# Kernel tuning notes

Hardware: AMD Instinct MI355X
Metric: run time of the kernel (lower is better)

The kernel has to match this reference:

```python
import jax, jax.numpy as jnp
import numpy as np

B, TE, TD, H = 8, 512, 256, 256  # batch, enc len, dec len, hidden (He==Hd)

def setup_inputs() -> dict:
    key = jax.random.key(0)
    k1, k2, k3, k4, k5 = jax.random.split(key, 5)
    # Keras 'uniform' initializer: U(-0.05, 0.05)
    u = lambda k, s: jax.random.uniform(k, s, jnp.float32, -0.05, 0.05)
    return {
        "encoder_out_seq": jax.random.normal(k1, (B, TE, H), jnp.float32),
        "decoder_out_seq": jax.random.normal(k2, (B, TD, H), jnp.float32),
        "W_a": u(k3, (H, H)),
        "U_a": u(k4, (H, H)),
        "V_a": u(k5, (H, 1)),
    }

def reference(encoder_out_seq, decoder_out_seq, W_a, U_a, V_a):
    # Bahdanau additive attention, fully batched (same math as the per-step K.rnn loop)
    We = jnp.einsum('bih,hk->bik', encoder_out_seq, W_a)   # [B,Te,H]
    Uh = jnp.einsum('bjh,hk->bjk', decoder_out_seq, U_a)   # [B,Td,H]
    # energies: V_a^T tanh(We_i + Uh_j)  -> [B,Td,Te]
    t = jnp.tanh(We[:, None, :, :] + Uh[:, :, None, :])    # [B,Td,Te,H]
    e = jnp.einsum('bjih,h->bji', t, V_a[:, 0])             # [B,Td,Te]
    e = jax.nn.softmax(e, axis=-1)                          # softmax over encoder positions
    c = jnp.einsum('bji,bih->bjh', e, encoder_out_seq)      # [B,Td,H]
    return (c, e)
```

## Files before the change

### kernel.cpp

```cpp
#include <hip/hip_runtime.h>


#define BB 8
#define TE 512
#define TD 256
#define HH 256

#define EXP2F(x) __builtin_amdgcn_exp2f(x)
#define RCPF(x)  __builtin_amdgcn_rcpf(x)
#define KSCALE   2.8853900817779268f
#define NSC      (-2.8853900817779268f)

typedef _Float16 h4 __attribute__((ext_vector_type(4)));
typedef _Float16 h8 __attribute__((ext_vector_type(8)));

__global__ __launch_bounds__(256) void k_pre(
    const float* __restrict__ enc, const float* __restrict__ dec,
    const float* __restrict__ Wa,  const float* __restrict__ Ua,
    _Float16* __restrict__ W4h, float* __restrict__ Uhe,
    _Float16* __restrict__ enc16)
{
    const int tid = threadIdx.x;

    if (blockIdx.x >= 384) {
        const size_t base = (size_t)(blockIdx.x - 384) * 16384;
        #pragma unroll 4
        for (int t = 0; t < 16; t++) {
            size_t idx = base + ((size_t)t * 256 + tid) * 4;
            float4 v = *(const float4*)(enc + idx);
            h4 o; o.x = (_Float16)v.x; o.y = (_Float16)v.y;
            o.z = (_Float16)v.z; o.w = (_Float16)v.w;
            *(h4*)(enc16 + idx) = o;
        }
        return;
    }

    const bool is_enc = blockIdx.x < 256;
    const int bi = is_enc ? blockIdx.x : (blockIdx.x - 256);
    const int m0 = (bi >> 2) * 64;
    const int n0 = (bi & 3) * 64;
    const float* X = is_enc ? enc : dec;
    const float* W = is_enc ? Wa : Ua;

    __shared__ float Xs[32][68];
    __shared__ float Ws[32][68];

    const int kq = tid & 7,  xr = tid >> 3;
    const int wk = tid >> 3, wn = (tid & 7) * 8;
    const int tx = tid & 15, ty = tid >> 4;

    float acc[4][4];
    #pragma unroll
    for (int r = 0; r < 4; r++)
        #pragma unroll
        for (int c = 0; c < 4; c++) acc[r][c] = 0.f;

    for (int kc = 0; kc < HH; kc += 32) {
        float4 xa = *(const float4*)(X + (size_t)(m0 + xr) * HH + kc + kq * 4);
        float4 xb = *(const float4*)(X + (size_t)(m0 + xr + 32) * HH + kc + kq * 4);
        float4 wa = *(const float4*)(W + (size_t)(kc + wk) * HH + n0 + wn);
        float4 wb = *(const float4*)(W + (size_t)(kc + wk) * HH + n0 + wn + 4);
        __syncthreads();
        Xs[kq * 4 + 0][xr] = xa.x; Xs[kq * 4 + 1][xr] = xa.y;
        Xs[kq * 4 + 2][xr] = xa.z; Xs[kq * 4 + 3][xr] = xa.w;
        Xs[kq * 4 + 0][xr + 32] = xb.x; Xs[kq * 4 + 1][xr + 32] = xb.y;
        Xs[kq * 4 + 2][xr + 32] = xb.z; Xs[kq * 4 + 3][xr + 32] = xb.w;
        *(float4*)&Ws[wk][wn]     = wa;
        *(float4*)&Ws[wk][wn + 4] = wb;
        __syncthreads();
        #pragma unroll
        for (int k = 0; k < 32; k++) {
            float4 a = *(const float4*)&Xs[k][ty * 4];
            float4 b = *(const float4*)&Ws[k][tx * 4];
            acc[0][0] = fmaf(a.x, b.x, acc[0][0]); acc[0][1] = fmaf(a.x, b.y, acc[0][1]);
            acc[0][2] = fmaf(a.x, b.z, acc[0][2]); acc[0][3] = fmaf(a.x, b.w, acc[0][3]);
            acc[1][0] = fmaf(a.y, b.x, acc[1][0]); acc[1][1] = fmaf(a.y, b.y, acc[1][1]);
            acc[1][2] = fmaf(a.y, b.z, acc[1][2]); acc[1][3] = fmaf(a.y, b.w, acc[1][3]);
            acc[2][0] = fmaf(a.z, b.x, acc[2][0]); acc[2][1] = fmaf(a.z, b.y, acc[2][1]);
            acc[2][2] = fmaf(a.z, b.z, acc[2][2]); acc[2][3] = fmaf(a.z, b.w, acc[2][3]);
            acc[3][0] = fmaf(a.w, b.x, acc[3][0]); acc[3][1] = fmaf(a.w, b.y, acc[3][1]);
            acc[3][2] = fmaf(a.w, b.z, acc[3][2]); acc[3][3] = fmaf(a.w, b.w, acc[3][3]);
        }
    }

    if (is_enc) {
        const int b  = m0 >> 9;
        const int ib = (m0 & 511) + ty * 4;
        const int hh = n0 + tx * 4;
        const int o  = hh >> 3;
        const int hf = (hh & 7);
        #pragma unroll
        for (int r = 0; r < 4; r++) {
            h4 v;
            v.x = (_Float16)EXP2F(acc[r][0] * KSCALE);
            v.y = (_Float16)EXP2F(acc[r][1] * KSCALE);
            v.z = (_Float16)EXP2F(acc[r][2] * KSCALE);
            v.w = (_Float16)EXP2F(acc[r][3] * KSCALE);
            *(h4*)(W4h + (((size_t)b * 32 + o) * TE + ib + r) * 8 + hf) = v;
        }
    } else {
        #pragma unroll
        for (int r = 0; r < 4; r++) {
            float4 v;
            v.x = EXP2F(acc[r][0] * KSCALE); v.y = EXP2F(acc[r][1] * KSCALE);
            v.z = EXP2F(acc[r][2] * KSCALE); v.w = EXP2F(acc[r][3] * KSCALE);
            *(float4*)(Uhe + (size_t)(m0 + ty * 4 + r) * HH + n0 + tx * 4) = v;
        }
    }
}

__global__ __launch_bounds__(512) void k_attn(
    const _Float16* __restrict__ enc16, const _Float16* __restrict__ W4h,
    const float* __restrict__ Uhe, const float* __restrict__ Va,
    float* __restrict__ out_c, float* __restrict__ out_e)
{
    const int wv = threadIdx.x >> 6, lane = threadIdx.x & 63;
    const int b   = blockIdx.x & 7;
    const int j0  = (blockIdx.x >> 3) * 4;
    const int jj0 = b * TD + j0;

    __shared__ float sP[4][TE];
    __shared__ float sR[8][4][HH];

    const int i = (wv << 6) + lane;
    const _Float16* wp = W4h + ((size_t)b * 32 * TE + i) * 8;
    const float* ua = Uhe + (size_t)jj0 * HH;
    const float* va = Va;

    float a0 = 0.f, a1 = 0.f, a2 = 0.f, a3 = 0.f;

#define OSTEP(ACC, UA, UB)                                                \
    {                                                                     \
        float A0 = fmaf(w0, (UA).x, 1.f);                                 \
        float A1 = fmaf(w1, (UA).y, 1.f);                                 \
        float A2 = fmaf(w2, (UA).z, 1.f);                                 \
        float A3 = fmaf(w3, (UA).w, 1.f);                                 \
        float A4 = fmaf(w4, (UB).x, 1.f);                                 \
        float A5 = fmaf(w5, (UB).y, 1.f);                                 \
        float A6 = fmaf(w6, (UB).z, 1.f);                                 \
        float A7 = fmaf(w7, (UB).w, 1.f);                                 \
        float dab = A0 * A1, dcd = A2 * A3;                               \
        float def_ = A4 * A5, dgh = A6 * A7;                              \
        float nab = fmaf(v4a.x, A1, v4a.y * A0);                          \
        float ncd = fmaf(v4a.z, A3, v4a.w * A2);                          \
        float nef = fmaf(v4b.x, A5, v4b.y * A4);                          \
        float ngh = fmaf(v4b.z, A7, v4b.w * A6);                          \
        float den4a = dab * dcd,  den4b = def_ * dgh;                     \
        float num4a = fmaf(nab, dcd, ncd * dab);                          \
        float num4b = fmaf(nef, dgh, ngh * def_);                         \
        float num = fmaf(num4a, den4b, num4b * den4a);                    \
        ACC = fmaf(num, RCPF(den4a * den4b), ACC);                        \
    }

    #pragma unroll 2
    for (int q = 0; q < 32; q++) {
        h8 w8 = *(const h8*)(wp + (size_t)q * TE * 8);
        float w0 = (float)w8[0], w1 = (float)w8[1];
        float w2 = (float)w8[2], w3 = (float)w8[3];
        float w4 = (float)w8[4], w5 = (float)w8[5];
        float w6 = (float)w8[6], w7 = (float)w8[7];
        float4 v4a = *(const float4*)(va + 8 * q);
        float4 v4b = *(const float4*)(va + 8 * q + 4);
        float4 u0a = *(const float4*)(ua + 8 * q);
        float4 u0b = *(const float4*)(ua + 8 * q + 4);
        float4 u1a = *(const float4*)(ua + HH + 8 * q);
        float4 u1b = *(const float4*)(ua + HH + 8 * q + 4);
        float4 u2a = *(const float4*)(ua + 2 * HH + 8 * q);
        float4 u2b = *(const float4*)(ua + 2 * HH + 8 * q + 4);
        float4 u3a = *(const float4*)(ua + 3 * HH + 8 * q);
        float4 u3b = *(const float4*)(ua + 3 * HH + 8 * q + 4);
        OSTEP(a0, u0a, u0b)
        OSTEP(a1, u1a, u1b)
        OSTEP(a2, u2a, u2b)
        OSTEP(a3, u3a, u3b)
    }
#undef OSTEP

    sP[0][i] = NSC * a0;
    sP[1][i] = NSC * a1;
    sP[2][i] = NSC * a2;
    sP[3][i] = NSC * a3;
    __syncthreads();

    if (wv < 4) {
        float ev[8];
        float m = -3.0e38f;
        #pragma unroll
        for (int k = 0; k < 8; k++) {
            ev[k] = sP[wv][lane + 64 * k];
            m = fmaxf(m, ev[k]);
        }
        #pragma unroll
        for (int off = 32; off; off >>= 1) m = fmaxf(m, __shfl_xor(m, off, 64));
        float s = 0.f;
        #pragma unroll
        for (int k = 0; k < 8; k++) { ev[k] = EXP2F(ev[k] - m); s += ev[k]; }
        #pragma unroll
        for (int off = 32; off; off >>= 1) s += __shfl_xor(s, off, 64);
        float rs = RCPF(s);
        float* oe = out_e + (size_t)(jj0 + wv) * TE;
        #pragma unroll
        for (int k = 0; k < 8; k++) {
            float p = ev[k] * rs;
            sP[wv][lane + 64 * k] = p;
            oe[lane + 64 * k] = p;
        }
    }
    __syncthreads();

    const int ib = wv << 6;
    const _Float16* eb = enc16 + ((size_t)b * TE + ib) * HH + 4 * lane;
    float4 c0 = {0,0,0,0}, c1 = {0,0,0,0}, c2 = {0,0,0,0}, c3 = {0,0,0,0};
    #pragma unroll 2
    for (int k = 0; k < 64; k++) {
        float p0 = sP[0][ib + k];
        float p1 = sP[1][ib + k];
        float p2 = sP[2][ib + k];
        float p3 = sP[3][ib + k];
        h4 q16 = *(const h4*)(eb + (size_t)k * HH);
        float qx = (float)q16.x, qy = (float)q16.y;
        float qz = (float)q16.z, qw = (float)q16.w;
        c0.x = fmaf(p0, qx, c0.x); c0.y = fmaf(p0, qy, c0.y);
        c0.z = fmaf(p0, qz, c0.z); c0.w = fmaf(p0, qw, c0.w);
        c1.x = fmaf(p1, qx, c1.x); c1.y = fmaf(p1, qy, c1.y);
        c1.z = fmaf(p1, qz, c1.z); c1.w = fmaf(p1, qw, c1.w);
        c2.x = fmaf(p2, qx, c2.x); c2.y = fmaf(p2, qy, c2.y);
        c2.z = fmaf(p2, qz, c2.z); c2.w = fmaf(p2, qw, c2.w);
        c3.x = fmaf(p3, qx, c3.x); c3.y = fmaf(p3, qy, c3.y);
        c3.z = fmaf(p3, qz, c3.z); c3.w = fmaf(p3, qw, c3.w);
    }
    *(float4*)&sR[wv][0][4 * lane] = c0;
    *(float4*)&sR[wv][1][4 * lane] = c1;
    *(float4*)&sR[wv][2][4 * lane] = c2;
    *(float4*)&sR[wv][3][4 * lane] = c3;
    __syncthreads();

    {
        const int jr = wv & 3;
        const int h2 = (wv >> 2) * 128 + 2 * lane;
        float sx = 0.f, sy = 0.f;
        #pragma unroll
        for (int ww = 0; ww < 8; ww++) {
            float2 t = *(const float2*)&sR[ww][jr][h2];
            sx += t.x; sy += t.y;
        }
        float2 o; o.x = sx; o.y = sy;
        *(float2*)(out_c + (size_t)(jj0 + jr) * HH + h2) = o;
    }
}

extern "C" void kernel_launch(void* const* d_in, const int* in_sizes, int n_in,
                              void* d_out, int out_size, void* d_ws, size_t ws_size,
                              hipStream_t stream) {
    const float* enc = (const float*)d_in[0];
    const float* dec = (const float*)d_in[1];
    const float* Wa  = (const float*)d_in[2];
    const float* Ua  = (const float*)d_in[3];
    const float* Va  = (const float*)d_in[4];

    _Float16* W4h   = (_Float16*)d_ws;
    _Float16* enc16 = W4h + (size_t)BB * HH * TE;
    float*    Uhe   = (float*)(enc16 + (size_t)BB * TE * HH);

    float* out_c = (float*)d_out;
    float* out_e = out_c + (size_t)BB * TD * HH;

    k_pre<<<448, 256, 0, stream>>>(enc, dec, Wa, Ua, W4h, Uhe, enc16);
    k_attn<<<BB * TD / 4, 512, 0, stream>>>(enc16, W4h, Uhe, Va, out_c, out_e);
}
```

Baseline: 114.9 us.

## Drop fp16 encoder copy, read fp32 directly, prefetch W4h and vectorize context loop

Removes the enc16 conversion blocks from the preprocessing kernel, so the context matmul reads fp32 encoder rows directly. The context loop now loads four probabilities per shared-memory read and four encoder rows per iteration. The energy loop software-prefetches the next four W4h vectors into registers, and launch bounds request four blocks per CU. In exchange, k_attn reads twice as many encoder bytes and needs more registers.

```diff
diff --git a/kernel.cpp b/kernel.cpp
--- a/kernel.cpp
+++ b/kernel.cpp
@@ -17,24 +17,9 @@
 __global__ __launch_bounds__(256) void k_pre(
     const float* __restrict__ enc, const float* __restrict__ dec,
     const float* __restrict__ Wa,  const float* __restrict__ Ua,
-    _Float16* __restrict__ W4h, float* __restrict__ Uhe,
-    _Float16* __restrict__ enc16)
+    _Float16* __restrict__ W4h, float* __restrict__ Uhe)
 {
     const int tid = threadIdx.x;
-
-    if (blockIdx.x >= 384) {
-        const size_t base = (size_t)(blockIdx.x - 384) * 16384;
-        #pragma unroll 4
-        for (int t = 0; t < 16; t++) {
-            size_t idx = base + ((size_t)t * 256 + tid) * 4;
-            float4 v = *(const float4*)(enc + idx);
-            h4 o; o.x = (_Float16)v.x; o.y = (_Float16)v.y;
-            o.z = (_Float16)v.z; o.w = (_Float16)v.w;
-            *(h4*)(enc16 + idx) = o;
-        }
-        return;
-    }
-
     const bool is_enc = blockIdx.x < 256;
     const int bi = is_enc ? blockIdx.x : (blockIdx.x - 256);
     const int m0 = (bi >> 2) * 64;
@@ -109,8 +94,8 @@
     }
 }
 
-__global__ __launch_bounds__(512) void k_attn(
-    const _Float16* __restrict__ enc16, const _Float16* __restrict__ W4h,
+__global__ __launch_bounds__(512, 4) void k_attn(
+    const float* __restrict__ enc, const _Float16* __restrict__ W4h,
     const float* __restrict__ Uhe, const float* __restrict__ Va,
     float* __restrict__ out_c, float* __restrict__ out_e)
 {
@@ -152,27 +137,43 @@
         ACC = fmaf(num, RCPF(den4a * den4b), ACC);                        \
     }
 
-    #pragma unroll 2
-    for (int q = 0; q < 32; q++) {
-        h8 w8 = *(const h8*)(wp + (size_t)q * TE * 8);
-        float w0 = (float)w8[0], w1 = (float)w8[1];
-        float w2 = (float)w8[2], w3 = (float)w8[3];
-        float w4 = (float)w8[4], w5 = (float)w8[5];
-        float w6 = (float)w8[6], w7 = (float)w8[7];
-        float4 v4a = *(const float4*)(va + 8 * q);
-        float4 v4b = *(const float4*)(va + 8 * q + 4);
-        float4 u0a = *(const float4*)(ua + 8 * q);
-        float4 u0b = *(const float4*)(ua + 8 * q + 4);
-        float4 u1a = *(const float4*)(ua + HH + 8 * q);
-        float4 u1b = *(const float4*)(ua + HH + 8 * q + 4);
-        float4 u2a = *(const float4*)(ua + 2 * HH + 8 * q);
-        float4 u2b = *(const float4*)(ua + 2 * HH + 8 * q + 4);
-        float4 u3a = *(const float4*)(ua + 3 * HH + 8 * q);
-        float4 u3b = *(const float4*)(ua + 3 * HH + 8 * q + 4);
-        OSTEP(a0, u0a, u0b)
-        OSTEP(a1, u1a, u1b)
-        OSTEP(a2, u2a, u2b)
-        OSTEP(a3, u3a, u3b)
+    h8 w_pf[4];
+    #pragma unroll
+    for (int k = 0; k < 4; k++)
+        w_pf[k] = *(const h8*)(wp + (size_t)k * TE * 8);
+
+    #pragma unroll
+    for (int q0 = 0; q0 < 32; q0 += 4) {
+        h8 wg[4];
+        #pragma unroll
+        for (int k = 0; k < 4; k++) wg[k] = w_pf[k];
+        #pragma unroll
+        for (int k = 0; k < 4; k++) {
+            int qq = q0 + 4 + k; if (qq > 31) qq = 31;
+            w_pf[k] = *(const h8*)(wp + (size_t)qq * TE * 8);
+        }
+        #pragma unroll
+        for (int k = 0; k < 4; k++) {
+            const int q = q0 + k;
+            float w0 = (float)wg[k][0], w1 = (float)wg[k][1];
+            float w2 = (float)wg[k][2], w3 = (float)wg[k][3];
+            float w4 = (float)wg[k][4], w5 = (float)wg[k][5];
+            float w6 = (float)wg[k][6], w7 = (float)wg[k][7];
+            float4 v4a = *(const float4*)(va + 8 * q);
+            float4 v4b = *(const float4*)(va + 8 * q + 4);
+            float4 u0a = *(const float4*)(ua + 8 * q);
+            float4 u0b = *(const float4*)(ua + 8 * q + 4);
+            float4 u1a = *(const float4*)(ua + HH + 8 * q);
+            float4 u1b = *(const float4*)(ua + HH + 8 * q + 4);
+            float4 u2a = *(const float4*)(ua + 2 * HH + 8 * q);
+            float4 u2b = *(const float4*)(ua + 2 * HH + 8 * q + 4);
+            float4 u3a = *(const float4*)(ua + 3 * HH + 8 * q);
+            float4 u3b = *(const float4*)(ua + 3 * HH + 8 * q + 4);
+            OSTEP(a0, u0a, u0b)
+            OSTEP(a1, u1a, u1b)
+            OSTEP(a2, u2a, u2b)
+            OSTEP(a3, u3a, u3b)
+        }
     }
 #undef OSTEP
 
@@ -209,25 +210,51 @@
     __syncthreads();
 
     const int ib = wv << 6;
-    const _Float16* eb = enc16 + ((size_t)b * TE + ib) * HH + 4 * lane;
+    const float* eb = enc + ((size_t)b * TE + ib) * HH + 4 * lane;
     float4 c0 = {0,0,0,0}, c1 = {0,0,0,0}, c2 = {0,0,0,0}, c3 = {0,0,0,0};
     #pragma unroll 2
-    for (int k = 0; k < 64; k++) {
-        float p0 = sP[0][ib + k];
-        float p1 = sP[1][ib + k];
-        float p2 = sP[2][ib + k];
-        float p3 = sP[3][ib + k];
-        h4 q16 = *(const h4*)(eb + (size_t)k * HH);
-        float qx = (float)q16.x, qy = (float)q16.y;
-        float qz = (float)q16.z, qw = (float)q16.w;
-        c0.x = fmaf(p0, qx, c0.x); c0.y = fmaf(p0, qy, c0.y);
-        c0.z = fmaf(p0, qz, c0.z); c0.w = fmaf(p0, qw, c0.w);
-        c1.x = fmaf(p1, qx, c1.x); c1.y = fmaf(p1, qy, c1.y);
-        c1.z = fmaf(p1, qz, c1.z); c1.w = fmaf(p1, qw, c1.w);
-        c2.x = fmaf(p2, qx, c2.x); c2.y = fmaf(p2, qy, c2.y);
-        c2.z = fmaf(p2, qz, c2.z); c2.w = fmaf(p2, qw, c2.w);
-        c3.x = fmaf(p3, qx, c3.x); c3.y = fmaf(p3, qy, c3.y);
-        c3.z = fmaf(p3, qz, c3.z); c3.w = fmaf(p3, qw, c3.w);
+    for (int k4 = 0; k4 < 16; k4++) {
+        float4 p0 = *(const float4*)&sP[0][ib + 4 * k4];
+        float4 p1 = *(const float4*)&sP[1][ib + 4 * k4];
+        float4 p2 = *(const float4*)&sP[2][ib + 4 * k4];
+        float4 p3 = *(const float4*)&sP[3][ib + 4 * k4];
+        const float* ep = eb + (size_t)k4 * 4 * HH;
+        float4 q0 = *(const float4*)(ep);
+        float4 q1 = *(const float4*)(ep + HH);
+        float4 q2 = *(const float4*)(ep + 2 * HH);
+        float4 q3 = *(const float4*)(ep + 3 * HH);
+        c0.x = fmaf(p0.x, q0.x, c0.x); c0.y = fmaf(p0.x, q0.y, c0.y);
+        c0.z = fmaf(p0.x, q0.z, c0.z); c0.w = fmaf(p0.x, q0.w, c0.w);
+        c1.x = fmaf(p1.x, q0.x, c1.x); c1.y = fmaf(p1.x, q0.y, c1.y);
+        c1.z = fmaf(p1.x, q0.z, c1.z); c1.w = fmaf(p1.x, q0.w, c1.w);
+        c2.x = fmaf(p2.x, q0.x, c2.x); c2.y = fmaf(p2.x, q0.y, c2.y);
+        c2.z = fmaf(p2.x, q0.z, c2.z); c2.w = fmaf(p2.x, q0.w, c2.w);
+        c3.x = fmaf(p3.x, q0.x, c3.x); c3.y = fmaf(p3.x, q0.y, c3.y);
+        c3.z = fmaf(p3.x, q0.z, c3.z); c3.w = fmaf(p3.x, q0.w, c3.w);
+        c0.x = fmaf(p0.y, q1.x, c0.x); c0.y = fmaf(p0.y, q1.y, c0.y);
+        c0.z = fmaf(p0.y, q1.z, c0.z); c0.w = fmaf(p0.y, q1.w, c0.w);
+        c1.x = fmaf(p1.y, q1.x, c1.x); c1.y = fmaf(p1.y, q1.y, c1.y);
+        c1.z = fmaf(p1.y, q1.z, c1.z); c1.w = fmaf(p1.y, q1.w, c1.w);
+        c2.x = fmaf(p2.y, q1.x, c2.x); c2.y = fmaf(p2.y, q1.y, c2.y);
+        c2.z = fmaf(p2.y, q1.z, c2.z); c2.w = fmaf(p2.y, q1.w, c2.w);
+        c3.x = fmaf(p3.y, q1.x, c3.x); c3.y = fmaf(p3.y, q1.y, c3.y);
+        c3.z = fmaf(p3.y, q1.z, c3.z); c3.w = fmaf(p3.y, q1.w, c3.w);
+        c0.x = fmaf(p0.z, q2.x, c0.x); c0.y = fmaf(p0.z, q2.y, c0.y);
+        c0.z = fmaf(p0.z, q2.z, c0.z); c0.w = fmaf(p0.z, q2.w, c0.w);
+        c1.x = fmaf(p1.z, q2.x, c1.x); c1.y = fmaf(p1.z, q2.y, c1.y);
+        c1.z = fmaf(p1.z, q2.z, c1.z); c1.w = fmaf(p1.z, q2.w, c1.w);
+        c2.x = fmaf(p2.z, q2.x, c2.x); c2.y = fmaf(p2.z, q2.y, c2.y);
+        c2.z = fmaf(p2.z, q2.z, c2.z); c2.w = fmaf(p2.z, q2.w, c2.w);
+        c3.x = fmaf(p3.z, q2.x, c3.x); c3.y = fmaf(p3.z, q2.y, c3.y);
+        c3.z = fmaf(p3.z, q2.z, c3.z); c3.w = fmaf(p3.z, q2.w, c3.w);
+        c0.x = fmaf(p0.w, q3.x, c0.x); c0.y = fmaf(p0.w, q3.y, c0.y);
+        c0.z = fmaf(p0.w, q3.z, c0.z); c0.w = fmaf(p0.w, q3.w, c0.w);
+        c1.x = fmaf(p1.w, q3.x, c1.x); c1.y = fmaf(p1.w, q3.y, c1.y);
+        c1.z = fmaf(p1.w, q3.z, c1.z); c1.w = fmaf(p1.w, q3.w, c1.w);
+        c2.x = fmaf(p2.w, q3.x, c2.x); c2.y = fmaf(p2.w, q3.y, c2.y);
+        c2.z = fmaf(p2.w, q3.z, c2.z); c2.w = fmaf(p2.w, q3.w, c2.w);
+        c3.x = fmaf(p3.w, q3.x, c3.x); c3.y = fmaf(p3.w, q3.y, c3.y);
+        c3.z = fmaf(p3.w, q3.z, c3.z); c3.w = fmaf(p3.w, q3.w, c3.w);
     }
     *(float4*)&sR[wv][0][4 * lane] = c0;
     *(float4*)&sR[wv][1][4 * lane] = c1;
@@ -258,13 +285,12 @@
     const float* Ua  = (const float*)d_in[3];
     const float* Va  = (const float*)d_in[4];
 
-    _Float16* W4h   = (_Float16*)d_ws;
-    _Float16* enc16 = W4h + (size_t)BB * HH * TE;
-    float*    Uhe   = (float*)(enc16 + (size_t)BB * TE * HH);
+    _Float16* W4h = (_Float16*)d_ws;
+    float*    Uhe = (float*)(W4h + (size_t)BB * HH * TE);
 
     float* out_c = (float*)d_out;
     float* out_e = out_c + (size_t)BB * TD * HH;
 
-    k_pre<<<448, 256, 0, stream>>>(enc, dec, Wa, Ua, W4h, Uhe, enc16);
-    k_attn<<<BB * TD / 4, 512, 0, stream>>>(enc16, W4h, Uhe, Va, out_c, out_e);
+    k_pre<<<384, 256, 0, stream>>>(enc, dec, Wa, Ua, W4h, Uhe);
+    k_attn<<<BB * TD / 4, 512, 0, stream>>>(enc, W4h, Uhe, Va, out_c, out_e);
 }
```

After: 119.1 us. +3.7%, slower.
